# Kernel tuning notes

Measured on AMD Instinct MI355X. Metric: run time of the kernel, lower is better.

Reference implementation:

```python
import jax, jax.numpy as jnp
import numpy as np

BATCH, L, DIM = 2, 2048, 1024
NST, DC, EXP = 16, 4, 2
DI = DIM * EXP


def setup_inputs() -> dict:
    key = jax.random.key(0)
    ks = jax.random.split(key, 8)
    x = jax.random.normal(ks[0], (BATCH, L, DIM), jnp.float32)
    in_proj_w = jax.random.normal(ks[1], (2 * DI, DIM), jnp.float32) * 0.02
    conv_w = jax.random.normal(ks[2], (DI, 1, DC), jnp.float32) * 0.1
    conv_b = jnp.zeros((DI,), jnp.float32)
    x_proj_w = jax.random.normal(ks[3], (2 * NST + 1, DI), jnp.float32) * 0.02
    dt_w = jax.random.normal(ks[4], (DI, 1), jnp.float32) * 0.5
    dt_b = jax.random.normal(ks[5], (DI,), jnp.float32) * 0.5 - 2.0
    # A initialized as log(1..d_state) broadcast over d_inner (as in __init__)
    A_log = jnp.log(jnp.broadcast_to(jnp.arange(1, NST + 1, dtype=jnp.float32), (DI, NST)))
    D_param = jnp.ones((DI,), jnp.float32)
    out_proj_w = jax.random.normal(ks[6], (DIM, DI), jnp.float32) * 0.02
    return dict(x=x, in_proj_w=in_proj_w, conv_w=conv_w, conv_b=conv_b,
                x_proj_w=x_proj_w, dt_w=dt_w, dt_b=dt_b, A_log=A_log,
                D_param=D_param, out_proj_w=out_proj_w)


def _silu(v):
    return v * jax.nn.sigmoid(v)


def _selective_scan(u, delta, A, Bp, Cp, D_param):
    # u, delta: (B, L, DI); A: (DI, N); Bp, Cp: (B, L, N); D_param: (DI,)
    delta = jax.nn.softplus(delta)
    d_seq = jnp.moveaxis(delta, 1, 0)  # (L, B, DI)
    u_seq = jnp.moveaxis(u, 1, 0)      # (L, B, DI)
    b_seq = jnp.moveaxis(Bp, 1, 0)     # (L, B, N)
    c_seq = jnp.moveaxis(Cp, 1, 0)     # (L, B, N)

    def step(h, inp):
        d, ut, bt, ct = inp  # (B,DI), (B,DI), (B,N), (B,N)
        dA = jnp.exp(d[..., None] * A[None])              # (B, DI, N)
        h = dA * h + (d * ut)[..., None] * bt[:, None, :]  # (B, DI, N)
        y = jnp.einsum('bdn,bn->bd', h, ct)               # (B, DI)
        return h, y

    h0 = jnp.zeros((u.shape[0], u.shape[2], A.shape[1]), u.dtype)
    _, ys = jax.lax.scan(step, h0, (d_seq, u_seq, b_seq, c_seq))
    y = jnp.moveaxis(ys, 0, 1)  # (B, L, DI)
    return y + D_param[None, None, :] * u


def reference(x, in_proj_w, conv_w, conv_b, x_proj_w, dt_w, dt_b, A_log, D_param, out_proj_w):
    Bb, Lq, _ = x.shape
    di = conv_w.shape[0]
    n = A_log.shape[1]
    # input projection -> split into x_inner and gate z
    xz = x @ in_proj_w.T                     # (B, L, 2*DI)
    x_inner, z = xz[..., :di], xz[..., di:]
    # causal depthwise conv1d (left pad d_conv-1)
    xc = jnp.transpose(x_inner, (0, 2, 1))   # (B, DI, L)
    xc = jax.lax.conv_general_dilated(
        xc, conv_w, window_strides=(1,), padding=[(DC - 1, 0)],
        feature_group_count=di, dimension_numbers=('NCH', 'OIH', 'NCH'))
    xc = xc + conv_b[None, :, None]
    xc = _silu(xc)                            # (B, DI, L)
    x_for_ssm = jnp.transpose(xc, (0, 2, 1))  # (B, L, DI)
    # SSM parameter projection
    ssm = x_for_ssm @ x_proj_w.T              # (B, L, 2N+1)
    dt_raw = ssm[..., :1]
    Bp = ssm[..., 1:1 + n]
    Cp = ssm[..., 1 + n:]
    dt = dt_raw @ dt_w.T + dt_b               # (B, L, DI)
    A = -jnp.exp(A_log)
    y = _selective_scan(x_for_ssm, dt, A, Bp, Cp, D_param)  # (B, L, DI)
    y = y * _silu(z)
    return y @ out_proj_w.T                   # (B, L, dim)
```

## Files before the change

kernel.cpp:

```cpp
#include <hip/hip_runtime.h>
#include <math.h>

#define BATCH 2
#define LSEQ  2048
#define DIMX  1024
#define NSTATE 16
#define DCONV 4
#define DI    2048
#define CHUNK 64
#define NCH   (LSEQ / CHUNK)
#define BL    (BATCH * LSEQ)
#define PJ    128

typedef __attribute__((ext_vector_type(8))) short short8;
typedef __attribute__((ext_vector_type(4))) float f32x4;

__device__ __forceinline__ unsigned short f2bf(float f) {
    unsigned int u = __float_as_uint(f);
    u += 0x7FFFu + ((u >> 16) & 1u);
    return (unsigned short)(u >> 16);
}
__device__ __forceinline__ ushort4 f2bf4(float4 v) {
    ushort4 o;
    o.x = f2bf(v.x); o.y = f2bf(v.y); o.z = f2bf(v.z); o.w = f2bf(v.w);
    return o;
}
__device__ __forceinline__ float bf2f(unsigned short b) {
    return __uint_as_float(((unsigned int)b) << 16);
}

#define R0 (BL * DIMX / 4)
#define R1 (2 * DI * DIMX / 4)
#define R2 (PJ * DI / 4)
__global__ __launch_bounds__(256) void cvt_front(
    const float* __restrict__ x, const float* __restrict__ w_in,
    const float* __restrict__ xpw,
    unsigned short* __restrict__ xbf, unsigned short* __restrict__ wbf_in,
    unsigned short* __restrict__ wpj)
{
    int i = blockIdx.x * 256 + threadIdx.x;
    if (i < R0) {
        ((ushort4*)xbf)[i] = f2bf4(((const float4*)x)[i]);
    } else if (i < R0 + R1) {
        int j = i - R0;
        ((ushort4*)wbf_in)[j] = f2bf4(((const float4*)w_in)[j]);
    } else {
        int j = i - R0 - R1;
        int row = (j * 4) >> 11;
        ushort4 o = {0, 0, 0, 0};
        if (row < 33) o = f2bf4(((const float4*)xpw)[j]);
        ((ushort4*)wpj)[j] = o;
    }
}

__global__ __launch_bounds__(256) void reduce4(
    const float* __restrict__ part, float* __restrict__ dst)
{
    int i = blockIdx.x * 256 + threadIdx.x;
    const size_t S = (size_t)BL * PJ / 4;
    float4 a = ((const float4*)part)[i];
    float4 b = ((const float4*)part)[i + S];
    float4 c = ((const float4*)part)[i + 2 * S];
    float4 d = ((const float4*)part)[i + 3 * S];
    float4 o;
    o.x = a.x + b.x + c.x + d.x;
    o.y = a.y + b.y + c.y + d.y;
    o.z = a.z + b.z + c.z + d.z;
    o.w = a.w + b.w + c.w + d.w;
    ((float4*)dst)[i] = o;
}

__global__ __launch_bounds__(256) void reduce2(
    const float* __restrict__ part, float* __restrict__ dst)
{
    int i = blockIdx.x * 256 + threadIdx.x;
    const size_t S = (size_t)BL * DIMX / 4;
    float4 a = ((const float4*)part)[i];
    float4 b = ((const float4*)part)[i + S];
    float4 o;
    o.x = a.x + b.x; o.y = a.y + b.y; o.z = a.z + b.z; o.w = a.w + b.w;
    ((float4*)dst)[i] = o;
}

__device__ __forceinline__ void pow_tree(float r, float p[16]) {
    p[0] = r;           p[1] = r * r;
    p[2] = p[1] * r;    p[3] = p[1] * p[1];
    p[4] = p[3] * p[0]; p[5] = p[3] * p[1];
    p[6] = p[3] * p[2]; p[7] = p[3] * p[3];
    p[8]  = p[7] * p[0]; p[9]  = p[7] * p[1];
    p[10] = p[7] * p[2]; p[11] = p[7] * p[3];
    p[12] = p[7] * p[4]; p[13] = p[7] * p[5];
    p[14] = p[7] * p[6]; p[15] = p[7] * p[7];
}

__global__ __launch_bounds__(256) void gemm_bf16_nt(
    const unsigned short* __restrict__ A, const unsigned short* __restrict__ Bw,
    float* __restrict__ C, int ldc, int K, int kLen, size_t cSlice)
{
    __shared__ unsigned short As[128 * 64];
    __shared__ unsigned short Bs[128 * 64];

    const int tid = threadIdx.x;
    const int wid = tid >> 6;
    const int lane = tid & 63;
    const int bm = blockIdx.y * 128;
    const int bn = blockIdx.x * 128;
    const int wm = (wid >> 1) * 64;
    const int wn = (wid & 1) * 64;
    const int kbeg = blockIdx.z * kLen;
    const int kend = kbeg + kLen;
    C += (size_t)blockIdx.z * cSlice;

    f32x4 acc[4][4];
    #pragma unroll
    for (int m = 0; m < 4; ++m)
        #pragma unroll
        for (int n = 0; n < 4; ++n) acc[m][n] = 0.0f;

    int rowS[4], colS[4];
    #pragma unroll
    for (int i = 0; i < 4; ++i) {
        int o = i * 4096 + wid * 1024 + lane * 16;
        int r = o >> 7;
        int cb = o & 127;
        rowS[i] = r;
        colS[i] = (cb ^ ((r & 7) << 4)) >> 1;
    }

    const int fr = lane & 15;
    const int kq = (lane >> 4) * 16;

    for (int k0 = kbeg; k0 < kend; k0 += 64) {
        __syncthreads();
        #pragma unroll
        for (int i = 0; i < 4; ++i) {
            __builtin_amdgcn_global_load_lds(
                (const __attribute__((address_space(1))) void*)
                    (A + (size_t)(bm + rowS[i]) * K + k0 + colS[i]),
                (__attribute__((address_space(3))) void*)
                    ((char*)As + i * 4096 + wid * 1024), 16, 0, 0);
            __builtin_amdgcn_global_load_lds(
                (const __attribute__((address_space(1))) void*)
                    (Bw + (size_t)(bn + rowS[i]) * K + k0 + colS[i]),
                (__attribute__((address_space(3))) void*)
                    ((char*)Bs + i * 4096 + wid * 1024), 16, 0, 0);
        }
        __syncthreads();

        #pragma unroll
        for (int kk = 0; kk < 2; ++kk) {
            short8 af[4], bf[4];
            #pragma unroll
            for (int m = 0; m < 4; ++m) {
                int ra = wm + m * 16 + fr;
                af[m] = *(const short8*)((const char*)As + ra * 128 +
                                         ((kk * 64 + kq) ^ ((ra & 7) << 4)));
                int rb = wn + m * 16 + fr;
                bf[m] = *(const short8*)((const char*)Bs + rb * 128 +
                                         ((kk * 64 + kq) ^ ((rb & 7) << 4)));
            }
            #pragma unroll
            for (int m = 0; m < 4; ++m)
                #pragma unroll
                for (int n = 0; n < 4; ++n)
                    acc[m][n] = __builtin_amdgcn_mfma_f32_16x16x32_bf16(
                        af[m], bf[n], acc[m][n], 0, 0, 0);
        }
    }

    #pragma unroll
    for (int m = 0; m < 4; ++m) {
        #pragma unroll
        for (int n = 0; n < 4; ++n) {
            int row0 = bm + wm + m * 16 + (lane >> 4) * 4;
            int col = bn + wn + n * 16 + fr;
            #pragma unroll
            for (int j = 0; j < 4; ++j)
                C[(size_t)(row0 + j) * ldc + col] = acc[m][n][j];
        }
    }
}

__global__ __launch_bounds__(256) void conv_silu(
    const float* __restrict__ xz, const float* __restrict__ cw,
    const float* __restrict__ cb, unsigned short* __restrict__ u_bf)
{
    int idx = blockIdx.x * 256 + threadIdx.x;
    int d  = (idx & 511) * 4;
    int bl = idx >> 9;
    int l  = bl & (LSEQ - 1);

    float4 w0 = *(const float4*)(cw + (d + 0) * DCONV);
    float4 w1 = *(const float4*)(cw + (d + 1) * DCONV);
    float4 w2 = *(const float4*)(cw + (d + 2) * DCONV);
    float4 w3 = *(const float4*)(cw + (d + 3) * DCONV);
    float4 acc = *(const float4*)(cb + d);

    #pragma unroll
    for (int t = 0; t < DCONV; ++t) {
        int ll = l - (DCONV - 1) + t;
        if (ll >= 0) {
            float4 xv = *(const float4*)(xz + (size_t)(bl - (DCONV - 1) + t) * (2 * DI) + d);
            float wt0 = (t == 0) ? w0.x : (t == 1) ? w0.y : (t == 2) ? w0.z : w0.w;
            float wt1 = (t == 0) ? w1.x : (t == 1) ? w1.y : (t == 2) ? w1.z : w1.w;
            float wt2 = (t == 0) ? w2.x : (t == 1) ? w2.y : (t == 2) ? w2.z : w2.w;
            float wt3 = (t == 0) ? w3.x : (t == 1) ? w3.y : (t == 2) ? w3.z : w3.w;
            acc.x = fmaf(wt0, xv.x, acc.x);
            acc.y = fmaf(wt1, xv.y, acc.y);
            acc.z = fmaf(wt2, xv.z, acc.z);
            acc.w = fmaf(wt3, xv.w, acc.w);
        }
    }
    float4 s;
    s.x = acc.x * __builtin_amdgcn_rcpf(1.f + __expf(-acc.x));
    s.y = acc.y * __builtin_amdgcn_rcpf(1.f + __expf(-acc.y));
    s.z = acc.z * __builtin_amdgcn_rcpf(1.f + __expf(-acc.z));
    s.w = acc.w * __builtin_amdgcn_rcpf(1.f + __expf(-acc.w));
    *(ushort4*)(u_bf + (size_t)bl * DI + d) = f2bf4(s);
}

__global__ __launch_bounds__(256) void scan_pass1(
    const unsigned short* __restrict__ u_bf, const float* __restrict__ dtBC,
    const float* __restrict__ dt_w, const float* __restrict__ dt_b,
    const float* __restrict__ Dp,
    float* __restrict__ xz,
    float* __restrict__ Ssum, float* __restrict__ Hloc)
{
    __shared__ float sdt[CHUNK];
    __shared__ float sB[CHUNK][NSTATE];
    __shared__ float sC[CHUNK][NSTATE];

    const int tid = threadIdx.x;
    const int bx = blockIdx.x;
    const int dblk = bx & 7;
    const int c = (bx >> 3) & (NCH - 1);
    const int b = bx >> 8;
    const int d = dblk * 256 + tid;
    const size_t row0 = (size_t)b * LSEQ + (size_t)c * CHUNK;

    for (int idx = tid; idx < CHUNK * 33; idx += 256) {
        int l = idx / 33;
        int j = idx - l * 33;
        float v = dtBC[(row0 + l) * PJ + j];
        if (j == 0) sdt[l] = v;
        else if (j < 17) sB[l][j - 1] = v;
        else sC[l][j - 17] = v;
    }
    __syncthreads();

    const float dtw = dt_w[d];
    const float dtb = dt_b[d];
    const float Dd = Dp[d];

    float h[NSTATE];
    #pragma unroll
    for (int n = 0; n < NSTATE; ++n) h[n] = 0.f;
    float S = 0.f;

    for (int l = 0; l < CHUNK; ++l) {
        float u = bf2f(u_bf[(row0 + l) * DI + d]);
        float pre = fmaf(sdt[l], dtw, dtb);
        float e = __expf(pre);
        float o = 1.f + e;
        float dt = (pre > 20.f) ? pre : __logf(o);
        float r = __builtin_amdgcn_rcpf(o);
        S += dt;
        float p[16];
        pow_tree(r, p);
        float dtu = dt * u;
        #pragma unroll
        for (int n = 0; n < NSTATE; ++n)
            h[n] = fmaf(p[n], h[n], dtu * sB[l][n]);
        float ya = h[0] * sC[l][0];
        float yb = h[1] * sC[l][1];
        float yc2 = h[2] * sC[l][2];
        float yd = h[3] * sC[l][3];
        #pragma unroll
        for (int n = 4; n < NSTATE; n += 4) {
            ya  = fmaf(h[n + 0], sC[l][n + 0], ya);
            yb  = fmaf(h[n + 1], sC[l][n + 1], yb);
            yc2 = fmaf(h[n + 2], sC[l][n + 2], yc2);
            yd  = fmaf(h[n + 3], sC[l][n + 3], yd);
        }
        float y = fmaf(Dd, u, (ya + yb) + (yc2 + yd));
        xz[(row0 + l) * (2 * DI) + d] = y;
    }

    Ssum[((size_t)b * NCH + c) * DI + d] = S;
    #pragma unroll
    for (int n = 0; n < NSTATE; ++n)
        Hloc[(((size_t)b * NCH + c) * NSTATE + n) * DI + d] = h[n];
}

__global__ __launch_bounds__(256) void combine_and_cvt(
    const float* __restrict__ Ssum, float* __restrict__ Hloc,
    const float* __restrict__ opw, unsigned short* __restrict__ wbf_out)
{
    const int bx = blockIdx.x;
    if (bx < 2048) {
        int i = bx * 256 + threadIdx.x;
        ((ushort4*)wbf_out)[i] = f2bf4(((const float4*)opw)[i]);
        return;
    }
    const int t = (bx - 2048) * 256 + threadIdx.x;
    const int d = t & (DI - 1);
    const int n = (t >> 11) & (NSTATE - 1);
    const int b = t >> 15;
    const float np1 = (float)(n + 1);

    float h = 0.f;
    for (int c = 0; c < NCH; ++c) {
        float S = Ssum[((size_t)b * NCH + c) * DI + d];
        size_t idx = (((size_t)b * NCH + c) * NSTATE + n) * DI + d;
        float loc = Hloc[idx];
        Hloc[idx] = h;
        h = fmaf(__expf(-S * np1), h, loc);
    }
}

__global__ __launch_bounds__(256) void scan_pass3(
    const float* __restrict__ dtBC,
    const float* __restrict__ dt_w, const float* __restrict__ dt_b,
    const float* __restrict__ Hin,
    const float* __restrict__ xz,
    unsigned short* __restrict__ ybf)
{
    __shared__ float sdt[CHUNK];
    __shared__ float sC[CHUNK][NSTATE];

    const int tid = threadIdx.x;
    const int bx = blockIdx.x;
    const int dblk = bx & 7;
    const int c = (bx >> 3) & (NCH - 1);
    const int b = bx >> 8;
    const int d = dblk * 256 + tid;
    const size_t row0 = (size_t)b * LSEQ + (size_t)c * CHUNK;

    for (int idx = tid; idx < CHUNK * 17; idx += 256) {
        int l = idx / 17;
        int j = idx - l * 17;
        float v = dtBC[(row0 + l) * PJ + ((j == 0) ? 0 : (16 + j))];
        if (j == 0) sdt[l] = v;
        else sC[l][j - 1] = v;
    }
    __syncthreads();

    const float dtw = dt_w[d];
    const float dtb = dt_b[d];

    float hin[NSTATE];
    #pragma unroll
    for (int n = 0; n < NSTATE; ++n)
        hin[n] = Hin[(((size_t)b * NCH + c) * NSTATE + n) * DI + d];

    float q = 1.f;
    for (int l = 0; l < CHUNK; ++l) {
        float pre = fmaf(sdt[l], dtw, dtb);
        float r = __builtin_amdgcn_rcpf(1.f + __expf(pre));
        q *= r;
        float p[16];
        pow_tree(q, p);
        float ya = (p[0] * hin[0]) * sC[l][0];
        float yb = (p[1] * hin[1]) * sC[l][1];
        float yc2 = (p[2] * hin[2]) * sC[l][2];
        float yd = (p[3] * hin[3]) * sC[l][3];
        #pragma unroll
        for (int n = 4; n < NSTATE; n += 4) {
            ya  = fmaf(p[n + 0] * hin[n + 0], sC[l][n + 0], ya);
            yb  = fmaf(p[n + 1] * hin[n + 1], sC[l][n + 1], yb);
            yc2 = fmaf(p[n + 2] * hin[n + 2], sC[l][n + 2], yc2);
            yd  = fmaf(p[n + 3] * hin[n + 3], sC[l][n + 3], yd);
        }
        size_t o = (row0 + l) * (2 * DI) + d;
        float y = xz[o] + ((ya + yb) + (yc2 + yd));
        float zz = xz[o + DI];
        float gate = zz * __builtin_amdgcn_rcpf(1.f + __expf(-zz));
        ybf[(row0 + l) * DI + d] = f2bf(y * gate);
    }
}

extern "C" void kernel_launch(void* const* d_in, const int* in_sizes, int n_in,
                              void* d_out, int out_size, void* d_ws, size_t ws_size,
                              hipStream_t stream)
{
    const float* x         = (const float*)d_in[0];
    const float* in_proj_w = (const float*)d_in[1];
    const float* conv_w    = (const float*)d_in[2];
    const float* conv_b    = (const float*)d_in[3];
    const float* x_proj_w  = (const float*)d_in[4];
    const float* dt_w      = (const float*)d_in[5];
    const float* dt_b      = (const float*)d_in[6];
    const float* D_param   = (const float*)d_in[8];
    const float* out_proj_w= (const float*)d_in[9];
    float* out = (float*)d_out;
    (void)d_in[7];

    float* xz   = (float*)d_ws;
    float* region2 = xz + (size_t)BL * 2 * DI;
    float* dtBC = region2 + (size_t)BL * DI;
    float* dtBCp = dtBC + (size_t)BL * PJ;
    unsigned short* wpj = (unsigned short*)(dtBCp + 4 * (size_t)BL * PJ);

    unsigned short* xbf     = (unsigned short*)region2;
    unsigned short* wbf_in  = xbf + (size_t)BL * DIMX;
    unsigned short* u_bf    = (unsigned short*)region2;
    unsigned short* ybf     = u_bf + (size_t)BL * DI;
    unsigned short* wbf_out = (unsigned short*)dtBCp;
    float* gemm2p = xz;

    float* Ssum = (float*)d_out;
    float* Hloc = Ssum + (size_t)BATCH * NCH * DI;

    dim3 blk(256);

    cvt_front<<<(R0 + R1 + R2) / 256, blk, 0, stream>>>(
        x, in_proj_w, x_proj_w, xbf, wbf_in, wpj);

    gemm_bf16_nt<<<dim3(4096 / 128, BL / 128, 1), blk, 0, stream>>>(
        xbf, wbf_in, xz, 2 * DI, DIMX, DIMX, 0);

    conv_silu<<<(BL * DI) / 1024, blk, 0, stream>>>(xz, conv_w, conv_b, u_bf);

    gemm_bf16_nt<<<dim3(1, BL / 128, 4), blk, 0, stream>>>(
        u_bf, wpj, dtBCp, PJ, DI, DI / 4, (size_t)BL * PJ);
    reduce4<<<(BL * PJ) / 1024, blk, 0, stream>>>(dtBCp, dtBC);

    scan_pass1<<<BATCH * NCH * (DI / 256), blk, 0, stream>>>(
        u_bf, dtBC, dt_w, dt_b, D_param, xz, Ssum, Hloc);
    combine_and_cvt<<<2048 + (BATCH * NSTATE * DI) / 256, blk, 0, stream>>>(
        Ssum, Hloc, out_proj_w, wbf_out);
    scan_pass3<<<BATCH * NCH * (DI / 256), blk, 0, stream>>>(
        dtBC, dt_w, dt_b, Hloc, xz, ybf);

    gemm_bf16_nt<<<dim3(DIMX / 128, BL / 128, 2), blk, 0, stream>>>(
        ybf, wbf_out, gemm2p, DIMX, DI, DI / 2, (size_t)BL * DIMX);
    reduce2<<<(BL * DIMX) / 1024, blk, 0, stream>>>(gemm2p, out);
}
```

Baseline: 218.0 us.

## Use 256x256 tiled bf16 GEMM with async global-to-LDS double buffering for in_proj

Adds a new 512-thread GEMM kernel with 256x256 output tiles, XOR-swizzled LDS layout, and direct global_load_lds double-buffered staging. It replaces the 128x128 GEMM for the input projection (4096x4096x1024). The aim is more data reuse per tile and overlap of loads with MFMA work. The grid shrinks to 256 blocks, and the 128KB LDS footprint may limit occupancy.

```diff
diff --git a/kernel.cpp b/kernel.cpp
--- a/kernel.cpp
+++ b/kernel.cpp
@@ -93,6 +93,123 @@
     p[14] = p[7] * p[6]; p[15] = p[7] * p[7];
 }
 
+__global__ __launch_bounds__(512, 2) void gemm256_bf16_nt(
+    const unsigned short* __restrict__ A, const unsigned short* __restrict__ Bw,
+    float* __restrict__ C, int ldc, int K)
+{
+    __shared__ char lds[131072];
+    const int tid = threadIdx.x;
+    const int wid = tid >> 6;
+    const int lane = tid & 63;
+    const int bm = blockIdx.y * 256;
+    const int bn = blockIdx.x * 256;
+    const int wr = ((wid >> 2) & 1) * 128;
+    const int wc = (wid & 3) * 64;
+
+    const int rowOff = wid * 8 + (lane >> 3);
+    const int srcEl  = ((lane & 7) ^ (lane >> 3)) * 8;
+    const int fr = lane & 15;
+    const int kq = (lane >> 4) * 16;
+
+    const unsigned short* Ap = A + (size_t)bm * K;
+    const unsigned short* Bp = Bw + (size_t)bn * K;
+
+    f32x4 acc[8][4];
+    #pragma unroll
+    for (int m = 0; m < 8; ++m)
+        #pragma unroll
+        for (int n = 0; n < 4; ++n) acc[m][n] = 0.0f;
+
+#define STAGE_T(buf, k0) do {                                                  \
+    char* base_ = lds + (buf) * 65536;                                         \
+    _Pragma("unroll")                                                          \
+    for (int h_ = 0; h_ < 2; ++h_) {                                           \
+        _Pragma("unroll")                                                      \
+        for (int j_ = 0; j_ < 2; ++j_) {                                       \
+            int r_ = h_ * 128 + j_ * 64 + rowOff;                              \
+            __builtin_amdgcn_global_load_lds(                                  \
+                (const __attribute__((address_space(1))) void*)                \
+                    (Ap + (size_t)r_ * K + (k0) + srcEl),                      \
+                (__attribute__((address_space(3))) void*)                      \
+                    (base_ + h_ * 16384 + j_ * 8192 + wid * 1024), 16, 0, 0);  \
+            __builtin_amdgcn_global_load_lds(                                  \
+                (const __attribute__((address_space(1))) void*)                \
+                    (Bp + (size_t)r_ * K + (k0) + srcEl),                      \
+                (__attribute__((address_space(3))) void*)                      \
+                    (base_ + 32768 + h_ * 16384 + j_ * 8192 + wid * 1024),     \
+                16, 0, 0);                                                     \
+        }                                                                      \
+    }                                                                          \
+} while (0)
+
+    STAGE_T(0, 0);
+    STAGE_T(1, 64);
+
+    const int nt = K >> 6;
+    for (int t = 0; t < nt; ++t) {
+        const int cur = t & 1;
+        if (t + 1 < nt) {
+            asm volatile("s_waitcnt vmcnt(8)" ::: "memory");
+        } else {
+            asm volatile("s_waitcnt vmcnt(0)" ::: "memory");
+        }
+        __builtin_amdgcn_s_barrier();
+        asm volatile("" ::: "memory");
+
+        const char* Ab = lds + cur * 65536;
+        const char* Bb = Ab + 32768;
+
+        short8 bfrag[4][2];
+        #pragma unroll
+        for (int nf = 0; nf < 4; ++nf) {
+            int rb = wc + nf * 16 + fr;
+            #pragma unroll
+            for (int kk = 0; kk < 2; ++kk)
+                bfrag[nf][kk] = *(const short8*)(Bb + rb * 128 +
+                                ((kk * 64 + kq) ^ ((rb & 7) << 4)));
+        }
+        #pragma unroll
+        for (int mh = 0; mh < 2; ++mh) {
+            short8 af[4][2];
+            #pragma unroll
+            for (int mf = 0; mf < 4; ++mf) {
+                int ra = wr + (mh * 4 + mf) * 16 + fr;
+                #pragma unroll
+                for (int kk = 0; kk < 2; ++kk)
+                    af[mf][kk] = *(const short8*)(Ab + ra * 128 +
+                                 ((kk * 64 + kq) ^ ((ra & 7) << 4)));
+            }
+            __builtin_amdgcn_s_setprio(1);
+            #pragma unroll
+            for (int kk = 0; kk < 2; ++kk)
+                #pragma unroll
+                for (int mf = 0; mf < 4; ++mf)
+                    #pragma unroll
+                    for (int nf = 0; nf < 4; ++nf)
+                        acc[mh * 4 + mf][nf] = __builtin_amdgcn_mfma_f32_16x16x32_bf16(
+                            af[mf][kk], bfrag[nf][kk], acc[mh * 4 + mf][nf], 0, 0, 0);
+            __builtin_amdgcn_s_setprio(0);
+        }
+
+        __builtin_amdgcn_s_barrier();
+        asm volatile("" ::: "memory");
+        if (t + 2 < nt) STAGE_T(cur, (t + 2) * 64);
+    }
+
+    #pragma unroll
+    for (int mf = 0; mf < 8; ++mf) {
+        #pragma unroll
+        for (int nf = 0; nf < 4; ++nf) {
+            int row0 = bm + wr + mf * 16 + (lane >> 4) * 4;
+            int col = bn + wc + nf * 16 + fr;
+            #pragma unroll
+            for (int j = 0; j < 4; ++j)
+                C[(size_t)(row0 + j) * ldc + col] = acc[mf][nf][j];
+        }
+    }
+#undef STAGE_T
+}
+
 __global__ __launch_bounds__(256) void gemm_bf16_nt(
     const unsigned short* __restrict__ A, const unsigned short* __restrict__ Bw,
     float* __restrict__ C, int ldc, int K, int kLen, size_t cSlice)
@@ -416,8 +533,8 @@
     cvt_front<<<(R0 + R1 + R2) / 256, blk, 0, stream>>>(
         x, in_proj_w, x_proj_w, xbf, wbf_in, wpj);
 
-    gemm_bf16_nt<<<dim3(4096 / 128, BL / 128, 1), blk, 0, stream>>>(
-        xbf, wbf_in, xz, 2 * DI, DIMX, DIMX, 0);
+    gemm256_bf16_nt<<<dim3(4096 / 256, BL / 256), dim3(512), 0, stream>>>(
+        xbf, wbf_in, xz, 2 * DI, DIMX);
 
     conv_silu<<<(BL * DI) / 1024, blk, 0, stream>>>(xz, conv_w, conv_b, u_bf);
 
```

New measurement: 210.4 us. -3.5%, faster.
